# Optimization experiments

Hardware: AMD Instinct MI355X
Metric: run time of the kernel (lower is better)

## Reference

```python
import jax, jax.numpy as jnp
import numpy as np

B, T, D, U = 8, 1024, 128, 2048
LEAK = 0.5       # leak_rate
EXPONENT = 2     # PowerIndex exponent
POW_INDEX = 2    # square neurons whose index % POW_INDEX == 0


def setup_inputs() -> dict:
    key = jax.random.key(0)
    k1, k2, k3, k4 = jax.random.split(key, 4)
    inputs = jax.random.normal(k1, (B, T, D), dtype=jnp.float32)
    # input-to-reservoir weights (InputMatrix ~ scaled dense here)
    w_in = jax.random.normal(k2, (D, U), dtype=jnp.float32) * (1.0 / np.sqrt(D))
    b_in = jax.random.uniform(k3, (U,), dtype=jnp.float32, minval=-0.05, maxval=0.05)
    # reservoir kernel (ErdosRenyi sparse random; dense surrogate scaled to
    # spectral radius ~0.9 via 0.9/sqrt(U))
    w_res = jax.random.normal(k4, (U, U), dtype=jnp.float32) * (0.9 / np.sqrt(U))
    return {"inputs": inputs, "w_in": w_in, "b_in": b_in, "w_res": w_res}


def reference(inputs, w_in, b_in, w_res):
    # Leaky ESN recurrence scanned over time:
    a = jnp.asarray(LEAK, inputs.dtype)
    # Precompute the input projection for all timesteps in one big GEMM.
    proj = jnp.einsum('btd,du->btu', inputs, w_in) + b_in  # [B,T,U]

    def step(state, p_t):  # state: [B,U], p_t: [B,U]
        pre = p_t + state @ w_res
        new = (1.0 - a) * state + a * jnp.tanh(pre)
        return new, new

    s0 = jnp.zeros((inputs.shape[0], w_res.shape[0]), inputs.dtype)
    _, states = jax.lax.scan(step, s0, jnp.swapaxes(proj, 0, 1))  # [T,B,U]
    states = jnp.swapaxes(states, 0, 1)  # [B,T,U]

    # PowerIndex: raise neurons at every POW_INDEX-th position to EXPONENT
    idx = jnp.arange(states.shape[-1])
    powered = jnp.where(idx % POW_INDEX == 0, states ** EXPONENT, states)

    # raw=False: concat input with reservoir output along features
    return jnp.concatenate([inputs, powered], axis=-1)  # [B,T,D+U]
```

## Files before the change

kernel.cpp:

```cpp
#include <hip/hip_runtime.h>
#include <cmath>

typedef __attribute__((ext_vector_type(8))) short short8;
typedef __attribute__((ext_vector_type(4))) float f32x4;
typedef unsigned long long u64;
typedef unsigned int u32;

#define RS 2208

__device__ __forceinline__ unsigned short f2bf(float x){
  u32 u = __float_as_uint(x);
  u32 r = u + 0x7FFFu + ((u >> 16) & 1u);
  return (unsigned short)(r >> 16);
}

__device__ __forceinline__ float tanh_fast(float x){
  float xc = fminf(fmaxf(x, -10.f), 10.f);
  float e = __expf(2.f * xc);
  return (e - 1.f) / (e + 1.f);
}

__global__ void bswz_kernel(const float* __restrict__ wres,
                            const float* __restrict__ win,
                            unsigned short* __restrict__ B){
  int tid = blockIdx.x * 256 + threadIdx.x;
  int l   = tid & 63;
  int cf  = tid >> 6;
  int f   = cf % 34;
  int gk  = cf / 34;
  int ks  = gk & 1;
  int gcg = gk >> 1;
  int col = (gcg << 4) + (l & 15);
  int k0  = ks * 1088 + (f << 5) + ((l >> 4) << 3);
  short8 vv;
  #pragma unroll
  for (int j = 0; j < 8; ++j){
    int k = k0 + j;
    float v = (k < 2048) ? wres[(size_t)k * 2048 + col]
                         : win[(size_t)(k - 2048) * 2048 + col];
    vv[j] = (short)f2bf(v);
  }
  *((short8*)(B + (size_t)tid * 8)) = vv;
}

__global__ void copy_in_kernel(const float* __restrict__ in, float* __restrict__ out){
  int i = blockIdx.x * 256 + threadIdx.x;
  int bt = i >> 5;
  int d4 = i & 31;
  float4 v = ((const float4*)in)[i];
  ((float4*)(out + (size_t)bt * 2176))[d4] = v;
}

__global__ void exinit_kernel(u64* __restrict__ ex){
  int i = blockIdx.x * 256 + threadIdx.x;
  ex[i] = (i < 4096) ? 0ULL : 0x0001000100010001ULL;
}

__global__ void __launch_bounds__(512, 2) esn_persist(
    const float* __restrict__ inputs,
    const float* __restrict__ b_in,
    const unsigned short* __restrict__ Bsw,
    u64* __restrict__ ex,
    float* __restrict__ out)
{
  __shared__ __align__(16) unsigned short As[2 * RS];
  __shared__ float red[2][4][16][2];

  const int tid = threadIdx.x;
  const int blk = blockIdx.x;
  const int r0  = (blk >> 5) << 1;
  const int cb  = blk & 31;
  const int wv  = tid >> 6;
  const int l   = tid & 63;
  const int m16 = l & 15;
  const int q   = l >> 4;
  const int cg  = wv >> 1;
  const int ks  = wv & 1;
  const int gcg = (cb << 2) + cg;
  const int colw0 = gcg << 4;

  short8 Bf[34];
  {
    const short8* bp = (const short8*)Bsw + (size_t)((gcg << 1) + ks) * 34 * 64 + l;
    #pragma unroll
    for (int f = 0; f < 34; ++f) Bf[f] = bp[f * 64];
  }
  const float bias = b_in[colw0 + m16];
  float s0 = 0.f, s1 = 0.f;

  const float* xr0 = inputs + (size_t)r0 * 1024 * 128;
  const u64 M = 0x0001000100010001ULL;

  for (int t = 0; t < 1024; ++t){
    if (tid < 64){
      const int row = tid >> 5;
      const int c   = tid & 31;
      float4 xv = ((const float4*)(xr0 + ((size_t)row * 1024 + t) * 128))[c];
      u64 pk = (u64)f2bf(xv.x) | ((u64)f2bf(xv.y) << 16)
             | ((u64)f2bf(xv.z) << 32) | ((u64)f2bf(xv.w) << 48);
      *((u64*)&As[row * RS + 2048 + (c << 2)]) = pk;
    }
    {
      u64* srcb = ex + ((size_t)(t & 1) * 8 + r0) * 512;
      const u64 wantm = ((t >> 1) & 1) ? M : 0ULL;
      u64 v0 = __hip_atomic_load(&srcb[tid],       __ATOMIC_RELAXED, __HIP_MEMORY_SCOPE_AGENT);
      u64 v1 = __hip_atomic_load(&srcb[512 + tid], __ATOMIC_RELAXED, __HIP_MEMORY_SCOPE_AGENT);
      u32 pend = 3;
      while (pend){
        u32 np = 0;
        if (pend & 1){
          if ((v0 & M) == wantm) *((u64*)&As[tid << 2]) = v0;
          else np |= 1;
        }
        if (pend & 2){
          if ((v1 & M) == wantm) *((u64*)&As[RS + (tid << 2)]) = v1;
          else np |= 2;
        }
        pend = np;
        if (pend & 1) v0 = __hip_atomic_load(&srcb[tid],       __ATOMIC_RELAXED, __HIP_MEMORY_SCOPE_AGENT);
        if (pend & 2) v1 = __hip_atomic_load(&srcb[512 + tid], __ATOMIC_RELAXED, __HIP_MEMORY_SCOPE_AGENT);
      }
    }
    __syncthreads();

    f32x4 acc0 = {0.f,0.f,0.f,0.f}, acc1 = {0.f,0.f,0.f,0.f};
    {
      const unsigned short* Ab = &As[(m16 & 1) * RS + ks * 1088 + (q << 3)];
      #pragma unroll
      for (int f = 0; f < 34; f += 2){
        short8 a0 = *((const short8*)(Ab + (f << 5)));
        short8 a1 = *((const short8*)(Ab + ((f + 1) << 5)));
        acc0 = __builtin_amdgcn_mfma_f32_16x16x32_bf16(a0, Bf[f],     acc0, 0, 0, 0);
        acc1 = __builtin_amdgcn_mfma_f32_16x16x32_bf16(a1, Bf[f + 1], acc1, 0, 0, 0);
      }
    }
    float p0 = acc0[0] + acc1[0];
    float p1 = acc0[1] + acc1[1];
    if (ks == 1 && l < 16){
      red[t & 1][cg][m16][0] = p0;
      red[t & 1][cg][m16][1] = p1;
    }
    __syncthreads();

    if (ks == 0 && l < 16){
      p0 += red[t & 1][cg][m16][0];
      p1 += red[t & 1][cg][m16][1];
      float nv0 = 0.5f * s0 + 0.5f * tanh_fast(p0 + bias);
      float nv1 = 0.5f * s1 + 0.5f * tanh_fast(p1 + bias);
      s0 = nv0; s1 = nv1;
      const u32 bit = (u32)(((t + 1) >> 1) & 1);
      u32 b0 = ((u32)f2bf(nv0) & 0xFFFEu) | bit;
      u32 b1 = ((u32)f2bf(nv1) & 0xFFFEu) | bit;
      u32 pr0 = b0 | (((u32)__shfl_xor((int)b0, 1)) << 16);
      u32 pr1 = b1 | (((u32)__shfl_xor((int)b1, 1)) << 16);
      u64 e0 = (u64)pr0 | ((u64)(u32)__shfl_xor((int)pr0, 2) << 32);
      u64 e1 = (u64)pr1 | ((u64)(u32)__shfl_xor((int)pr1, 2) << 32);
      const int u = colw0 + m16;
      if ((m16 & 3) == 0){
        u64* exw = ex + ((size_t)((t + 1) & 1) * 8 + r0) * 512;
        const int p = (colw0 + m16) >> 2;
        __hip_atomic_store(&exw[p],       e0, __ATOMIC_RELAXED, __HIP_MEMORY_SCOPE_AGENT);
        __hip_atomic_store(&exw[512 + p], e1, __ATOMIC_RELAXED, __HIP_MEMORY_SCOPE_AGENT);
      }
      float pw0 = (u & 1) ? nv0 : nv0 * nv0;
      float pw1 = (u & 1) ? nv1 : nv1 * nv1;
      out[((size_t)r0 * 1024 + t) * 2176 + 128 + u] = pw0;
      out[((size_t)(r0 + 1) * 1024 + t) * 2176 + 128 + u] = pw1;
    }
  }
}

extern "C" void kernel_launch(void* const* d_in, const int* in_sizes, int n_in,
                              void* d_out, int out_size, void* d_ws, size_t ws_size,
                              hipStream_t stream){
  const float* inputs = (const float*)d_in[0];
  const float* w_in   = (const float*)d_in[1];
  const float* b_in   = (const float*)d_in[2];
  const float* w_res  = (const float*)d_in[3];
  float* out = (float*)d_out;

  u64* ex = (u64*)d_ws;
  unsigned short* Bsw = (unsigned short*)((char*)d_ws + 65536);

  exinit_kernel<<<32, 256, 0, stream>>>(ex);
  bswz_kernel<<<2176, 256, 0, stream>>>(w_res, w_in, Bsw);
  copy_in_kernel<<<1024, 256, 0, stream>>>(inputs, out);
  esn_persist<<<128, 512, 0, stream>>>(inputs, b_in, Bsw, ex, out);
}
```

Measured before the change: 3.123 ms.

## Give each wave a private state copy and drop the block barrier before MFMA

```diff
diff --git a/kernel.cpp b/kernel.cpp
--- a/kernel.cpp
+++ b/kernel.cpp
@@ -6,7 +6,7 @@
 typedef unsigned long long u64;
 typedef unsigned int u32;
 
-#define RS 2208
+#define AG __ATOMIC_RELAXED, __HIP_MEMORY_SCOPE_AGENT
 
 __device__ __forceinline__ unsigned short f2bf(float x){
   u32 u = __float_as_uint(x);
@@ -63,7 +63,7 @@
     u64* __restrict__ ex,
     float* __restrict__ out)
 {
-  __shared__ __align__(16) unsigned short As[2 * RS];
+  __shared__ __align__(16) unsigned short As[8][2][1104];
   __shared__ float red[2][4][16][2];
 
   const int tid = threadIdx.x;
@@ -91,41 +91,65 @@
   const float* xr0 = inputs + (size_t)r0 * 1024 * 128;
   const u64 M = 0x0001000100010001ULL;
 
+  int eidx[5];
+  u32 pend0;
+  if (ks == 0){
+    eidx[0] = l; eidx[1] = l + 64; eidx[2] = l + 128; eidx[3] = l + 192;
+    eidx[4] = (l < 16) ? l + 256 : 0;
+    pend0 = (l < 16) ? 0x3FFu : 0x1EFu;
+  } else {
+    eidx[0] = 272 + l; eidx[1] = 336 + l; eidx[2] = 400 + l;
+    eidx[3] = (l < 48) ? 464 + l : 0;
+    eidx[4] = 0;
+    pend0 = (l < 48) ? 0x1EFu : 0x0E7u;
+  }
+
+  const int xrow = l >> 5, xc = l & 31;
+  float4 xv;
+  if (ks == 1) xv = ((const float4*)(xr0 + (size_t)xrow * 1024 * 128))[xc];
+
   for (int t = 0; t < 1024; ++t){
-    if (tid < 64){
-      const int row = tid >> 5;
-      const int c   = tid & 31;
-      float4 xv = ((const float4*)(xr0 + ((size_t)row * 1024 + t) * 128))[c];
+    if (ks == 1){
       u64 pk = (u64)f2bf(xv.x) | ((u64)f2bf(xv.y) << 16)
              | ((u64)f2bf(xv.z) << 32) | ((u64)f2bf(xv.w) << 48);
-      *((u64*)&As[row * RS + 2048 + (c << 2)]) = pk;
+      *((u64*)&As[wv][xrow][960 + (xc << 2)]) = pk;
+      if (t < 1023)
+        xv = ((const float4*)(xr0 + ((size_t)xrow * 1024 + t + 1) * 128))[xc];
     }
     {
       u64* srcb = ex + ((size_t)(t & 1) * 8 + r0) * 512;
-      const u64 wantm = ((t >> 1) & 1) ? M : 0ULL;
-      u64 v0 = __hip_atomic_load(&srcb[tid],       __ATOMIC_RELAXED, __HIP_MEMORY_SCOPE_AGENT);
-      u64 v1 = __hip_atomic_load(&srcb[512 + tid], __ATOMIC_RELAXED, __HIP_MEMORY_SCOPE_AGENT);
-      u32 pend = 3;
-      while (pend){
+      const u64 want = ((t >> 1) & 1) ? M : 0ULL;
+      u64 vb[10];
+      u32 pend = pend0;
+      #pragma unroll
+      for (int i = 0; i < 10; ++i)
+        if (pend & (1u << i))
+          vb[i] = __hip_atomic_load(&srcb[(i >= 5 ? 512 : 0) + eidx[i % 5]], AG);
+      for (;;){
         u32 np = 0;
-        if (pend & 1){
-          if ((v0 & M) == wantm) *((u64*)&As[tid << 2]) = v0;
-          else np |= 1;
-        }
-        if (pend & 2){
-          if ((v1 & M) == wantm) *((u64*)&As[RS + (tid << 2)]) = v1;
-          else np |= 2;
+        #pragma unroll
+        for (int i = 0; i < 10; ++i){
+          if (pend & (1u << i)){
+            if ((vb[i] & M) == want){
+              const int e   = eidx[i % 5];
+              const int row = (i >= 5);
+              const int kl  = (ks == 0) ? (e << 2) : ((e << 2) - 1088);
+              *((u64*)&As[wv][row][kl]) = vb[i];
+            } else np |= (1u << i);
+          }
         }
         pend = np;
-        if (pend & 1) v0 = __hip_atomic_load(&srcb[tid],       __ATOMIC_RELAXED, __HIP_MEMORY_SCOPE_AGENT);
-        if (pend & 2) v1 = __hip_atomic_load(&srcb[512 + tid], __ATOMIC_RELAXED, __HIP_MEMORY_SCOPE_AGENT);
+        if (!pend) break;
+        #pragma unroll
+        for (int i = 0; i < 10; ++i)
+          if (pend & (1u << i))
+            vb[i] = __hip_atomic_load(&srcb[(i >= 5 ? 512 : 0) + eidx[i % 5]], AG);
       }
     }
-    __syncthreads();
 
     f32x4 acc0 = {0.f,0.f,0.f,0.f}, acc1 = {0.f,0.f,0.f,0.f};
     {
-      const unsigned short* Ab = &As[(m16 & 1) * RS + ks * 1088 + (q << 3)];
+      const unsigned short* Ab = &As[wv][m16 & 1][q << 3];
       #pragma unroll
       for (int f = 0; f < 34; f += 2){
         short8 a0 = *((const short8*)(Ab + (f << 5)));
@@ -159,8 +183,8 @@
       if ((m16 & 3) == 0){
         u64* exw = ex + ((size_t)((t + 1) & 1) * 8 + r0) * 512;
         const int p = (colw0 + m16) >> 2;
-        __hip_atomic_store(&exw[p],       e0, __ATOMIC_RELAXED, __HIP_MEMORY_SCOPE_AGENT);
-        __hip_atomic_store(&exw[512 + p], e1, __ATOMIC_RELAXED, __HIP_MEMORY_SCOPE_AGENT);
+        __hip_atomic_store(&exw[p],       e0, AG);
+        __hip_atomic_store(&exw[512 + p], e1, AG);
       }
       float pw0 = (u & 1) ? nv0 : nv0 * nv0;
       float pw1 = (u & 1) ? nv1 : nv1 * nv1;
```

Measured after the change: 4.073 ms. 30.4% more time.
